# Kernel optimization log

Hardware: AMD Instinct MI355X
Metric: run time of the kernel (lower is better)

The kernel has to match this reference:

```python
import jax, jax.numpy as jnp
import numpy as np

EPS = 1e-5

def _conv1x1(x, w, b=None):
    # x: (B, Cin, H, W), w: (Cout, Cin) -> (B, Cout, H, W)
    y = jnp.einsum('bchw,oc->bohw', x, w)
    if b is not None:
        y = y + b[None, :, None, None]
    return y

def setup_inputs() -> dict:
    key = jax.random.key(0)
    ks = jax.random.split(key, 14)
    B, C, I = 4, 256, 128
    Ha = Wa = 64
    Hd = Wd = 128
    s = 0.05
    return {
        'detect':  jax.random.normal(ks[0], (B, C, Hd, Wd), jnp.float32),
        'aim':     jax.random.normal(ks[1], (B, C, Ha, Wa), jnp.float32),
        'g_w':     jax.random.normal(ks[2], (I, C), jnp.float32) * s,
        'g_b':     jax.random.normal(ks[3], (I,), jnp.float32) * s,
        'theta_w': jax.random.normal(ks[4], (I, C), jnp.float32) * s,
        'theta_b': jax.random.normal(ks[5], (I,), jnp.float32) * s,
        'phi_w':   jax.random.normal(ks[6], (I, C), jnp.float32) * s,
        'phi_b':   jax.random.normal(ks[7], (I,), jnp.float32) * s,
        'q_w':     jax.random.normal(ks[8], (C, I), jnp.float32) * s,
        'q_b':     jax.random.normal(ks[9], (C,), jnp.float32) * s,
        'bn_gamma': jax.random.normal(ks[10], (C,), jnp.float32),
        'bn_beta':  jax.random.normal(ks[11], (C,), jnp.float32),
        'bn_mean':  jax.random.normal(ks[12], (C,), jnp.float32),
        'bn_var':   jax.random.uniform(ks[13], (C,), jnp.float32) + 0.5,
    }

def reference(detect, aim, g_w, g_b, theta_w, theta_b, phi_w, phi_b,
              q_w, q_b, bn_gamma, bn_beta, bn_mean, bn_var):
    B, C, Hd, Wd = detect.shape
    _, _, Ha, Wa = aim.shape
    Na = Ha * Wa
    Nd = Hd * Wd
    I = g_w.shape[0]

    # 1x1 conv projections, flattened to token sequences
    a_g   = _conv1x1(aim, g_w, g_b).reshape(B, I, Na)        # g(aim)
    th_a  = _conv1x1(aim, theta_w, theta_b).reshape(B, I, Na)
    ph_d  = _conv1x1(detect, phi_w, phi_b).reshape(B, I, Nd)
    # (d_x = g(detect) is dead code in the original forward; omitted)

    # f = theta_x @ phi_x : (B, Na, Nd); permuted -> (B, Nd, Na); N = Na
    f = jnp.einsum('bia,bid->bad', th_a, ph_d)               # (B, Na, Nd)
    inv_n = jnp.float32(1.0 / Na)
    # non_det = (f^T / Na) @ a_x : (B, Nd, I) -> permute -> (B, I, Nd)
    non = jnp.einsum('bad,bia->bid', f * inv_n, a_g)         # (B, I, Nd)
    non = non.reshape(B, I, Hd, Wd)

    # Q: 1x1 conv (I -> C) + BatchNorm (inference mode, running stats)
    y = _conv1x1(non, q_w, q_b)
    inv_std = jax.lax.rsqrt(bn_var + EPS)
    y = (y - bn_mean[None, :, None, None]) * (bn_gamma * inv_std)[None, :, None, None] \
        + bn_beta[None, :, None, None]

    return y + detect
```

## Files before the change

### kernel.cpp

```cpp
#include <hip/hip_runtime.h>

constexpr int BB   = 4;
constexpr int CCH  = 256;
constexpr int IDIM = 128;
constexpr int NAa  = 4096;
constexpr int NDd  = 16384;
constexpr int PAD  = 320;
constexpr float NAinv = 1.0f / 4096.0f;

typedef __bf16 bf16x8 __attribute__((ext_vector_type(8)));
typedef float  f32x4  __attribute__((ext_vector_type(4)));

__device__ inline unsigned short f2bfu(float f) {
    unsigned u = __float_as_uint(f);
    u += 0x7FFFu + ((u >> 16) & 1u);
    return (unsigned short)(u >> 16);
}
__device__ inline float bf2f(unsigned short u) {
    return __uint_as_float((unsigned)u << 16);
}
__device__ inline bf16x8 cvt8(f32x4 a, f32x4 b) {
    union { bf16x8 v; unsigned short u[8]; } t;
    t.u[0] = f2bfu(a[0]); t.u[1] = f2bfu(a[1]); t.u[2] = f2bfu(a[2]); t.u[3] = f2bfu(a[3]);
    t.u[4] = f2bfu(b[0]); t.u[5] = f2bfu(b[1]); t.u[6] = f2bfu(b[2]); t.u[7] = f2bfu(b[3]);
    return t.v;
}
__device__ inline bf16x8 ld_cvt8(const float* p) {
    return cvt8(*(const f32x4*)p, *(const f32x4*)(p + 4));
}

__global__ __launch_bounds__(256) void k1(const float* __restrict__ aim,
                                          const float* __restrict__ qw,
                                          const float* __restrict__ gw,
                                          const float* __restrict__ gb,
                                          const float* __restrict__ thw,
                                          const float* __restrict__ thb,
                                          const float* __restrict__ phw,
                                          const float* __restrict__ phb,
                                          float* __restrict__ Spart,
                                          float* __restrict__ r,
                                          unsigned short* __restrict__ Ph,
                                          unsigned short* __restrict__ Rt) {
    __shared__ __align__(16) char sm[49152];
    const int bx = blockIdx.x, t = threadIdx.x;

    if (bx < 256) {
        const int b = bx >> 6, rem = bx & 63;
        const int tile = rem >> 2, kc = rem & 3;
        const int mb = (tile >> 2) * 64, nbb = (tile & 3) * 64;
        const float* A = aim + (long)b * CCH * NAa;
        const int w = t >> 6, lane = t & 63, quad = lane >> 4, l16 = lane & 15;
        f32x4 acc[4][4] = {};
        for (int ks = 0; ks < 8; ++ks) {
            const int k = kc * 1024 + w * 256 + ks * 32 + quad * 8;
            bf16x8 af[4], bfr[4];
            #pragma unroll
            for (int i = 0; i < 4; ++i) af[i]  = ld_cvt8(A + (long)(mb + i * 16 + l16) * NAa + k);
            #pragma unroll
            for (int j = 0; j < 4; ++j) bfr[j] = ld_cvt8(A + (long)(nbb + j * 16 + l16) * NAa + k);
            #pragma unroll
            for (int i = 0; i < 4; ++i)
                #pragma unroll
                for (int j = 0; j < 4; ++j)
                    acc[i][j] = __builtin_amdgcn_mfma_f32_16x16x32_bf16(af[i], bfr[j], acc[i][j], 0, 0, 0);
        }
        float* sred = (float*)sm;
        if (w > 0) {
            #pragma unroll
            for (int i = 0; i < 4; ++i)
                #pragma unroll
                for (int j = 0; j < 4; ++j)
                    #pragma unroll
                    for (int reg = 0; reg < 4; ++reg)
                        sred[(w - 1) * 4096 + ((i * 4 + j) * 4 + reg) * 64 + lane] = acc[i][j][reg];
        }
        __syncthreads();
        if (w == 0) {
            float* o = Spart + ((long)(b * 4 + kc)) * 65536;
            #pragma unroll
            for (int i = 0; i < 4; ++i)
                #pragma unroll
                for (int j = 0; j < 4; ++j)
                    #pragma unroll
                    for (int reg = 0; reg < 4; ++reg) {
                        float v = acc[i][j][reg];
                        #pragma unroll
                        for (int rg = 0; rg < 3; ++rg)
                            v += sred[rg * 4096 + ((i * 4 + j) * 4 + reg) * 64 + lane];
                        o[(long)(mb + i * 16 + quad * 4 + reg) * 256 + nbb + j * 16 + l16] = v;
                    }
        }
    } else if (bx < 272) {
        const int rid = bx - 256;
        const int w = t >> 6, lane = t & 63;
        for (int rr = 0; rr < 16; ++rr) {
            const int row = rid * 64 + w * 16 + rr;
            const float* src = aim + (long)row * NAa;
            float s = 0.f;
            #pragma unroll 4
            for (int q = 0; q < 16; ++q) {
                f32x4 v = *(const f32x4*)(src + q * 256 + lane * 4);
                s += v[0] + v[1] + v[2] + v[3];
            }
            #pragma unroll
            for (int off = 32; off > 0; off >>= 1) s += __shfl_down(s, off, 64);
            if (lane == 0) r[row] = s;
        }
    } else {
        const int idx = (bx - 272) * 256 + t;
        if (idx < CCH * PAD) {
            const int o = idx / PAD, c = idx - o * PAD;
            float acc = 0.f;
            if (c <= 256) {
                for (int i = 0; i < IDIM; ++i)
                    acc += qw[o * IDIM + i] * ((c < 256) ? gw[i * CCH + c] : gb[i]);
            }
            Ph[idx] = f2bfu(acc);
        } else {
            const int id2 = idx - CCH * PAD;
            const int c2 = id2 / PAD, k = id2 - c2 * PAD;
            float acc = 0.f;
            if (k <= 256 && c2 <= 256) {
                for (int i = 0; i < IDIM; ++i) {
                    const float av = (k < 256) ? thw[i * CCH + k] : thb[i];
                    const float bv = (c2 < 256) ? phw[i * CCH + c2] : phb[i];
                    acc += av * bv;
                }
            }
            Rt[id2] = f2bfu(acc);
        }
    }
}

__global__ __launch_bounds__(256) void k2(const float* __restrict__ Spart,
                                          const float* __restrict__ r,
                                          const unsigned short* __restrict__ Ph,
                                          const unsigned short* __restrict__ Rt,
                                          const float* __restrict__ qb,
                                          const float* __restrict__ gamma,
                                          const float* __restrict__ beta,
                                          const float* __restrict__ mean,
                                          const float* __restrict__ var,
                                          unsigned short* __restrict__ W5u,
                                          float* __restrict__ b5) {
    const int b = blockIdx.y, m0 = blockIdx.x * 64;
    const float* Sp = Spart + (long)b * 4 * 65536;
    const float* rb = r + b * CCH;
    const int t = threadIdx.x, w = t >> 6, lane = t & 63, quad = lane >> 4, l16 = lane & 15;
    __shared__ __align__(16) unsigned short M1[64][264];
    __shared__ float sv1[320], sv2[64];

    for (int c2 = t; c2 < 320; c2 += 256) {
        float s = 0.f;
        for (int kk = 0; kk < 256; kk += 4) {
            ushort4 u = *(const ushort4*)(Rt + (long)c2 * PAD + kk);
            s += rb[kk] * bf2f(u.x) + rb[kk + 1] * bf2f(u.y) + rb[kk + 2] * bf2f(u.z) + rb[kk + 3] * bf2f(u.w);
        }
        sv1[c2] = s;
    }
    if (t < 64) {
        const int o = m0 + t;
        float s = 0.f;
        for (int kk = 0; kk < 256; kk += 4) {
            ushort4 u = *(const ushort4*)(Ph + (long)o * PAD + kk);
            s += rb[kk] * bf2f(u.x) + rb[kk + 1] * bf2f(u.y) + rb[kk + 2] * bf2f(u.z) + rb[kk + 3] * bf2f(u.w);
        }
        sv2[t] = s;
    }

    {
        f32x4 acc[4][4] = {};
        for (int jt = 0; jt < 256; jt += 32) {
            bf16x8 af[4], bfr[4];
            #pragma unroll
            for (int i = 0; i < 4; ++i)
                af[i] = *(const bf16x8*)(Ph + (long)(m0 + i * 16 + l16) * PAD + jt + quad * 8);
            #pragma unroll
            for (int j = 0; j < 4; ++j) {
                const int row = w * 64 + j * 16 + l16;
                f32x4 s0 = {}, s1 = {};
                #pragma unroll
                for (int kc = 0; kc < 4; ++kc) {
                    const float* pp = Sp + (long)kc * 65536 + (long)row * 256 + jt + quad * 8;
                    s0 += *(const f32x4*)pp;
                    s1 += *(const f32x4*)(pp + 4);
                }
                bfr[j] = cvt8(s0, s1);
            }
            #pragma unroll
            for (int i = 0; i < 4; ++i)
                #pragma unroll
                for (int j = 0; j < 4; ++j)
                    acc[i][j] = __builtin_amdgcn_mfma_f32_16x16x32_bf16(af[i], bfr[j], acc[i][j], 0, 0, 0);
        }
        #pragma unroll
        for (int i = 0; i < 4; ++i)
            #pragma unroll
            for (int j = 0; j < 4; ++j)
                #pragma unroll
                for (int reg = 0; reg < 4; ++reg)
                    M1[i * 16 + quad * 4 + reg][w * 64 + j * 16 + l16] = f2bfu(acc[i][j][reg]);
    }
    __syncthreads();

    f32x4 acc[4][5] = {};
    for (int kt = 0; kt < 256; kt += 32) {
        bf16x8 af[4], bfr[5];
        #pragma unroll
        for (int i = 0; i < 4; ++i)
            af[i] = *(const bf16x8*)&M1[i * 16 + l16][kt + quad * 8];
        #pragma unroll
        for (int j = 0; j < 5; ++j)
            bfr[j] = *(const bf16x8*)(Rt + (long)(w * 80 + j * 16 + l16) * PAD + kt + quad * 8);
        #pragma unroll
        for (int i = 0; i < 4; ++i)
            #pragma unroll
            for (int j = 0; j < 5; ++j)
                acc[i][j] = __builtin_amdgcn_mfma_f32_16x16x32_bf16(af[i], bfr[j], acc[i][j], 0, 0, 0);
    }
    #pragma unroll
    for (int i = 0; i < 4; ++i) {
        #pragma unroll
        for (int reg = 0; reg < 4; ++reg) {
            const int o = m0 + i * 16 + quad * 4 + reg;
            const float ph256 = bf2f(Ph[(long)o * PAD + 256]);
            const float s = gamma[o] * rsqrtf(var[o] + 1e-5f);
            const float sv2v = sv2[i * 16 + quad * 4 + reg];
            #pragma unroll
            for (int j = 0; j < 5; ++j) {
                const int c2 = w * 80 + j * 16 + l16;
                const float rtc = bf2f(Rt[(long)c2 * PAD + 256]);
                const float core = acc[i][j][reg] + ph256 * sv1[c2] + (sv2v + ph256 * 4096.0f) * rtc;
                const float val = core * s * NAinv;
                if (c2 < CCH)
                    W5u[((long)b * CCH + o) * CCH + c2] = f2bfu(val + (o == c2 ? 1.0f : 0.0f));
                else if (c2 == CCH)
                    b5[b * CCH + o] = val + s * (qb[o] - mean[o]) + beta[o];
            }
        }
    }
}

__global__ __launch_bounds__(512) void k_final(const float* __restrict__ D0,
                                               const unsigned short* __restrict__ W5u,
                                               const float* __restrict__ b5,
                                               float* __restrict__ out) {
    const int z = blockIdx.z;
    const int nb = blockIdx.x * 128;
    const float* D = D0 + (long)z * CCH * NDd;
    float* O = out + (long)z * CCH * NDd;
    const unsigned short* W = W5u + (long)z * CCH * CCH;
    const int t = threadIdx.x, wv = t >> 6, lane = t & 63, quad = lane >> 4, l16 = lane & 15;
    const int mw = (wv >> 1) * 64, nw = (wv & 1) * 64;
    const int r2 = t >> 4, g = t & 15;
    const bool st = (t < 256);
    __shared__ __align__(16) unsigned short lb[2][128][40];

    f32x4 xa[4], xb[4];
    bf16x8 af[2][4], bfr[4];

    auto load_tile = [&](f32x4* x, int kt) {
        const float* base = D + (long)(kt + 2 * r2) * NDd + nb + 8 * g;
        x[0] = *(const f32x4*)(base);
        x[1] = *(const f32x4*)(base + NDd);
        x[2] = *(const f32x4*)(base + 4);
        x[3] = *(const f32x4*)(base + NDd + 4);
    };
    auto write_tile = [&](int buf, const f32x4* x) {
        #pragma unroll
        for (int e2 = 0; e2 < 2; ++e2)
            #pragma unroll
            for (int c = 0; c < 4; ++c) {
                const int n = 8 * g + 4 * e2 + c;
                const int p = ((n & 7) << 4) + (n >> 3);
                const unsigned v = (unsigned)f2bfu(x[2 * e2][c]) |
                                   ((unsigned)f2bfu(x[2 * e2 + 1][c]) << 16);
                *(unsigned*)&lb[buf][p][2 * r2] = v;
            }
    };
    auto loadW = [&](bf16x8* a, int kt) {
        #pragma unroll
        for (int i = 0; i < 4; ++i)
            a[i] = *(const bf16x8*)(W + (long)(mw + i * 16 + l16) * CCH + kt + quad * 8);
    };

    int pj[4];
    #pragma unroll
    for (int j = 0; j < 4; ++j) {
        const int n = nw + j * 16 + l16;
        pj[j] = ((n & 7) << 4) + (n >> 3);
    }

    f32x4 acc[4][4] = {};
    if (st) { load_tile(xa, 0); load_tile(xb, 32); }
    loadW(af[0], 0);
    if (st) { write_tile(0, xa); load_tile(xa, 64); }
    #pragma unroll
    for (int it = 0; it < 8; ++it) {
        __syncthreads();
        const int kt = it * 32;
        #pragma unroll
        for (int j = 0; j < 4; ++j)
            bfr[j] = *(const bf16x8*)&lb[it & 1][pj[j]][quad * 8];
        #pragma unroll
        for (int i = 0; i < 4; ++i)
            #pragma unroll
            for (int j = 0; j < 4; ++j)
                acc[i][j] = __builtin_amdgcn_mfma_f32_16x16x32_bf16(af[it & 1][i], bfr[j], acc[i][j], 0, 0, 0);
        if (it < 7) {
            loadW(af[(it + 1) & 1], kt + 32);
            if (st) {
                write_tile((it + 1) & 1, (it & 1) ? xa : xb);
                if (it < 5) load_tile((it & 1) ? xa : xb, (it + 3) * 32);
            }
        }
    }
    #pragma unroll
    for (int i = 0; i < 4; ++i) {
        float bv[4];
        #pragma unroll
        for (int reg = 0; reg < 4; ++reg)
            bv[reg] = b5[z * CCH + mw + i * 16 + quad * 4 + reg];
        #pragma unroll
        for (int j = 0; j < 4; ++j) {
            const int n = nb + nw + j * 16 + l16;
            #pragma unroll
            for (int reg = 0; reg < 4; ++reg)
                O[(long)(mw + i * 16 + quad * 4 + reg) * NDd + n] = acc[i][j][reg] + bv[reg];
        }
    }
}

extern "C" void kernel_launch(void* const* d_in, const int* in_sizes, int n_in,
                              void* d_out, int out_size, void* d_ws, size_t ws_size,
                              hipStream_t stream) {
    const float* detect = (const float*)d_in[0];
    const float* aim    = (const float*)d_in[1];
    const float* g_w    = (const float*)d_in[2];
    const float* g_b    = (const float*)d_in[3];
    const float* th_w   = (const float*)d_in[4];
    const float* th_b   = (const float*)d_in[5];
    const float* phi_w  = (const float*)d_in[6];
    const float* phi_b  = (const float*)d_in[7];
    const float* q_w    = (const float*)d_in[8];
    const float* q_b    = (const float*)d_in[9];
    const float* gamma  = (const float*)d_in[10];
    const float* beta   = (const float*)d_in[11];
    const float* mean   = (const float*)d_in[12];
    const float* var    = (const float*)d_in[13];
    float* out = (float*)d_out;

    float* ws = (float*)d_ws;
    float* Spart = ws;
    unsigned short* us = (unsigned short*)(Spart + 1048576);
    unsigned short* W5u     = us;
    unsigned short* Phat_u  = W5u + 262144;
    unsigned short* RhatT_u = Phat_u + 81920;
    float* r  = (float*)(RhatT_u + 102400);
    float* b5 = r + 1024;

    k1<<<dim3(992), dim3(256), 0, stream>>>(aim, q_w, g_w, g_b, th_w, th_b, phi_w, phi_b,
                                            Spart, r, Phat_u, RhatT_u);
    k2<<<dim3(4, BB), dim3(256), 0, stream>>>(Spart, r, Phat_u, RhatT_u, q_b, gamma, beta,
                                              mean, var, W5u, b5);
    k_final<<<dim3(NDd / 128, 1, BB), dim3(512), 0, stream>>>(detect, W5u, b5, out);
}
```

Before: 250.3 us.

## Split k2 into two wider-grid kernels with split-K wave reduction

The single k2 kernel (16 blocks) is split into k2a, which computes the M1 product over a 4x4 output tiling with the K dimension split across waves and reduced through shared memory, and also computes the sv1/sv2 vectors in separate blocks, and k2b, which runs the second product on an 80-block grid with the same split-K scheme and applies the epilogue. The aim is to raise parallelism in this small middle stage, which used only 16 workgroups. The cost is an extra kernel launch, a global round trip for M1 and the sv vectors, and shared-memory reductions.

```diff
diff --git a/kernel.cpp b/kernel.cpp
--- a/kernel.cpp
+++ b/kernel.cpp
@@ -132,52 +132,32 @@
     }
 }
 
-__global__ __launch_bounds__(256) void k2(const float* __restrict__ Spart,
-                                          const float* __restrict__ r,
-                                          const unsigned short* __restrict__ Ph,
-                                          const unsigned short* __restrict__ Rt,
-                                          const float* __restrict__ qb,
-                                          const float* __restrict__ gamma,
-                                          const float* __restrict__ beta,
-                                          const float* __restrict__ mean,
-                                          const float* __restrict__ var,
-                                          unsigned short* __restrict__ W5u,
-                                          float* __restrict__ b5) {
-    const int b = blockIdx.y, m0 = blockIdx.x * 64;
-    const float* Sp = Spart + (long)b * 4 * 65536;
-    const float* rb = r + b * CCH;
-    const int t = threadIdx.x, w = t >> 6, lane = t & 63, quad = lane >> 4, l16 = lane & 15;
-    __shared__ __align__(16) unsigned short M1[64][264];
-    __shared__ float sv1[320], sv2[64];
-
-    for (int c2 = t; c2 < 320; c2 += 256) {
-        float s = 0.f;
-        for (int kk = 0; kk < 256; kk += 4) {
-            ushort4 u = *(const ushort4*)(Rt + (long)c2 * PAD + kk);
-            s += rb[kk] * bf2f(u.x) + rb[kk + 1] * bf2f(u.y) + rb[kk + 2] * bf2f(u.z) + rb[kk + 3] * bf2f(u.w);
-        }
-        sv1[c2] = s;
-    }
-    if (t < 64) {
-        const int o = m0 + t;
-        float s = 0.f;
-        for (int kk = 0; kk < 256; kk += 4) {
-            ushort4 u = *(const ushort4*)(Ph + (long)o * PAD + kk);
-            s += rb[kk] * bf2f(u.x) + rb[kk + 1] * bf2f(u.y) + rb[kk + 2] * bf2f(u.z) + rb[kk + 3] * bf2f(u.w);
-        }
-        sv2[t] = s;
-    }
-
-    {
+__global__ __launch_bounds__(256) void k2a(const float* __restrict__ Spart,
+                                           const float* __restrict__ r,
+                                           const unsigned short* __restrict__ Ph,
+                                           const unsigned short* __restrict__ Rt,
+                                           unsigned short* __restrict__ M1g,
+                                           float* __restrict__ sv1,
+                                           float* __restrict__ sv2) {
+    __shared__ __align__(16) float sred[3 * 4096];
+    const int bx = blockIdx.x, t = threadIdx.x;
+
+    if (bx < 64) {
+        const int b = bx >> 4, rem = bx & 15;
+        const int m0 = (rem >> 2) * 64, n0 = (rem & 3) * 64;
+        const float* Sp = Spart + (long)b * 4 * 65536;
+        const int w = t >> 6, lane = t & 63, quad = lane >> 4, l16 = lane & 15;
         f32x4 acc[4][4] = {};
-        for (int jt = 0; jt < 256; jt += 32) {
+        #pragma unroll
+        for (int js = 0; js < 2; ++js) {
+            const int jt = w * 64 + js * 32;
             bf16x8 af[4], bfr[4];
             #pragma unroll
             for (int i = 0; i < 4; ++i)
                 af[i] = *(const bf16x8*)(Ph + (long)(m0 + i * 16 + l16) * PAD + jt + quad * 8);
             #pragma unroll
             for (int j = 0; j < 4; ++j) {
-                const int row = w * 64 + j * 16 + l16;
+                const int row = n0 + j * 16 + l16;
                 f32x4 s0 = {}, s1 = {};
                 #pragma unroll
                 for (int kc = 0; kc < 4; ++kc) {
@@ -193,49 +173,122 @@
                 for (int j = 0; j < 4; ++j)
                     acc[i][j] = __builtin_amdgcn_mfma_f32_16x16x32_bf16(af[i], bfr[j], acc[i][j], 0, 0, 0);
         }
+        if (w > 0) {
+            #pragma unroll
+            for (int i = 0; i < 4; ++i)
+                #pragma unroll
+                for (int j = 0; j < 4; ++j)
+                    #pragma unroll
+                    for (int reg = 0; reg < 4; ++reg)
+                        sred[(w - 1) * 4096 + ((i * 4 + j) * 4 + reg) * 64 + lane] = acc[i][j][reg];
+        }
+        __syncthreads();
+        if (w == 0) {
+            unsigned short* M = M1g + (long)b * 65536;
+            #pragma unroll
+            for (int i = 0; i < 4; ++i)
+                #pragma unroll
+                for (int j = 0; j < 4; ++j)
+                    #pragma unroll
+                    for (int reg = 0; reg < 4; ++reg) {
+                        float v = acc[i][j][reg];
+                        #pragma unroll
+                        for (int rg = 0; rg < 3; ++rg)
+                            v += sred[rg * 4096 + ((i * 4 + j) * 4 + reg) * 64 + lane];
+                        M[(long)(m0 + i * 16 + quad * 4 + reg) * 256 + n0 + j * 16 + l16] = f2bfu(v);
+                    }
+        }
+    } else {
+        const int b = bx - 64;
+        const float* rb = r + b * CCH;
+        for (int c2 = t; c2 < 320; c2 += 256) {
+            float s = 0.f;
+            for (int kk = 0; kk < 256; kk += 4) {
+                ushort4 u = *(const ushort4*)(Rt + (long)c2 * PAD + kk);
+                s += rb[kk] * bf2f(u.x) + rb[kk + 1] * bf2f(u.y) + rb[kk + 2] * bf2f(u.z) + rb[kk + 3] * bf2f(u.w);
+            }
+            sv1[b * 320 + c2] = s;
+        }
+        {
+            const int o = t;
+            float s = 0.f;
+            for (int kk = 0; kk < 256; kk += 4) {
+                ushort4 u = *(const ushort4*)(Ph + (long)o * PAD + kk);
+                s += rb[kk] * bf2f(u.x) + rb[kk + 1] * bf2f(u.y) + rb[kk + 2] * bf2f(u.z) + rb[kk + 3] * bf2f(u.w);
+            }
+            sv2[b * 256 + o] = s;
+        }
+    }
+}
+
+__global__ __launch_bounds__(256) void k2b(const unsigned short* __restrict__ M1g,
+                                           const float* __restrict__ sv1,
+                                           const float* __restrict__ sv2,
+                                           const unsigned short* __restrict__ Ph,
+                                           const unsigned short* __restrict__ Rt,
+                                           const float* __restrict__ qb,
+                                           const float* __restrict__ gamma,
+                                           const float* __restrict__ beta,
+                                           const float* __restrict__ mean,
+                                           const float* __restrict__ var,
+                                           unsigned short* __restrict__ W5u,
+                                           float* __restrict__ b5) {
+    __shared__ __align__(16) float sred[3 * 4096];
+    const int b = blockIdx.z, m0 = blockIdx.y * 64, n0 = blockIdx.x * 64;
+    const unsigned short* M = M1g + (long)b * 65536;
+    const int t = threadIdx.x, w = t >> 6, lane = t & 63, quad = lane >> 4, l16 = lane & 15;
+
+    f32x4 acc[4][4] = {};
+    #pragma unroll
+    for (int ks = 0; ks < 2; ++ks) {
+        const int kt = w * 64 + ks * 32;
+        bf16x8 af[4], bfr[4];
         #pragma unroll
         for (int i = 0; i < 4; ++i)
+            af[i] = *(const bf16x8*)(M + (long)(m0 + i * 16 + l16) * 256 + kt + quad * 8);
+        #pragma unroll
+        for (int j = 0; j < 4; ++j)
+            bfr[j] = *(const bf16x8*)(Rt + (long)(n0 + j * 16 + l16) * PAD + kt + quad * 8);
+        #pragma unroll
+        for (int i = 0; i < 4; ++i)
             #pragma unroll
             for (int j = 0; j < 4; ++j)
+                acc[i][j] = __builtin_amdgcn_mfma_f32_16x16x32_bf16(af[i], bfr[j], acc[i][j], 0, 0, 0);
+    }
+    if (w > 0) {
+        #pragma unroll
+        for (int i = 0; i < 4; ++i)
+            #pragma unroll
+            for (int j = 0; j < 4; ++j)
                 #pragma unroll
                 for (int reg = 0; reg < 4; ++reg)
-                    M1[i * 16 + quad * 4 + reg][w * 64 + j * 16 + l16] = f2bfu(acc[i][j][reg]);
+                    sred[(w - 1) * 4096 + ((i * 4 + j) * 4 + reg) * 64 + lane] = acc[i][j][reg];
     }
     __syncthreads();
-
-    f32x4 acc[4][5] = {};
-    for (int kt = 0; kt < 256; kt += 32) {
-        bf16x8 af[4], bfr[5];
-        #pragma unroll
-        for (int i = 0; i < 4; ++i)
-            af[i] = *(const bf16x8*)&M1[i * 16 + l16][kt + quad * 8];
-        #pragma unroll
-        for (int j = 0; j < 5; ++j)
-            bfr[j] = *(const bf16x8*)(Rt + (long)(w * 80 + j * 16 + l16) * PAD + kt + quad * 8);
-        #pragma unroll
-        for (int i = 0; i < 4; ++i)
-            #pragma unroll
-            for (int j = 0; j < 5; ++j)
-                acc[i][j] = __builtin_amdgcn_mfma_f32_16x16x32_bf16(af[i], bfr[j], acc[i][j], 0, 0, 0);
-    }
-    #pragma unroll
-    for (int i = 0; i < 4; ++i) {
-        #pragma unroll
-        for (int reg = 0; reg < 4; ++reg) {
-            const int o = m0 + i * 16 + quad * 4 + reg;
-            const float ph256 = bf2f(Ph[(long)o * PAD + 256]);
-            const float s = gamma[o] * rsqrtf(var[o] + 1e-5f);
-            const float sv2v = sv2[i * 16 + quad * 4 + reg];
-            #pragma unroll
-            for (int j = 0; j < 5; ++j) {
-                const int c2 = w * 80 + j * 16 + l16;
-                const float rtc = bf2f(Rt[(long)c2 * PAD + 256]);
-                const float core = acc[i][j][reg] + ph256 * sv1[c2] + (sv2v + ph256 * 4096.0f) * rtc;
-                const float val = core * s * NAinv;
-                if (c2 < CCH)
-                    W5u[((long)b * CCH + o) * CCH + c2] = f2bfu(val + (o == c2 ? 1.0f : 0.0f));
-                else if (c2 == CCH)
-                    b5[b * CCH + o] = val + s * (qb[o] - mean[o]) + beta[o];
+    if (w == 0) {
+        #pragma unroll
+        for (int i = 0; i < 4; ++i) {
+            #pragma unroll
+            for (int reg = 0; reg < 4; ++reg) {
+                const int o = m0 + i * 16 + quad * 4 + reg;
+                const float ph256 = bf2f(Ph[(long)o * PAD + 256]);
+                const float s = gamma[o] * rsqrtf(var[o] + 1e-5f);
+                const float sv2v = sv2[b * 256 + o];
+                #pragma unroll
+                for (int j = 0; j < 4; ++j) {
+                    const int c2 = n0 + j * 16 + l16;
+                    float v = acc[i][j][reg];
+                    #pragma unroll
+                    for (int rg = 0; rg < 3; ++rg)
+                        v += sred[rg * 4096 + ((i * 4 + j) * 4 + reg) * 64 + lane];
+                    const float rtc = bf2f(Rt[(long)c2 * PAD + 256]);
+                    const float core = v + ph256 * sv1[b * 320 + c2] + (sv2v + ph256 * 4096.0f) * rtc;
+                    const float val = core * s * NAinv;
+                    if (c2 < CCH)
+                        W5u[((long)b * CCH + o) * CCH + c2] = f2bfu(val + (o == c2 ? 1.0f : 0.0f));
+                    else if (c2 == CCH)
+                        b5[b * CCH + o] = val + s * (qb[o] - mean[o]) + beta[o];
+                }
             }
         }
     }
@@ -356,12 +409,16 @@
     unsigned short* W5u     = us;
     unsigned short* Phat_u  = W5u + 262144;
     unsigned short* RhatT_u = Phat_u + 81920;
-    float* r  = (float*)(RhatT_u + 102400);
-    float* b5 = r + 1024;
+    unsigned short* M1g     = RhatT_u + 102400;
+    float* r   = (float*)(M1g + 262144);
+    float* b5  = r + 1024;
+    float* sv1 = b5 + 1024;
+    float* sv2 = sv1 + 1280;
 
     k1<<<dim3(992), dim3(256), 0, stream>>>(aim, q_w, g_w, g_b, th_w, th_b, phi_w, phi_b,
                                             Spart, r, Phat_u, RhatT_u);
-    k2<<<dim3(4, BB), dim3(256), 0, stream>>>(Spart, r, Phat_u, RhatT_u, q_b, gamma, beta,
-                                              mean, var, W5u, b5);
+    k2a<<<dim3(68), dim3(256), 0, stream>>>(Spart, r, Phat_u, RhatT_u, M1g, sv1, sv2);
+    k2b<<<dim3(5, 4, BB), dim3(256), 0, stream>>>(M1g, sv1, sv2, Phat_u, RhatT_u, q_b,
+                                                  gamma, beta, mean, var, W5u, b5);
     k_final<<<dim3(NDd / 128, 1, BB), dim3(512), 0, stream>>>(detect, W5u, b5, out);
 }
```

Measured after the change: 220.9 us. -11.7%, faster.
